# Kernel tuning notes

Measured on AMD Instinct MI355X. Metric: run time of the kernel, lower is better.

The kernel has to match this reference:

```python
import jax, jax.numpy as jnp
import numpy as np

WINDOW = 5  # must be odd so conv 'same' output length == tlength


def setup_inputs() -> dict:
    key = jax.random.key(0)
    tlength = 16777216
    return {"factor": jax.random.normal(key, (tlength,), dtype=jnp.float32)}


def reference(factor):
    window = WINDOW
    # moving average: conv1d with ones kernel, padding=window//2 (== 'same' for odd window)
    w = jnp.ones((window,), dtype=factor.dtype)
    moving_average = jnp.convolve(factor, w, mode='same') / window
    # rate of change: 0 followed by squared consecutive differences
    diffs = (moving_average[:-1] - moving_average[1:]) ** 2
    change = jnp.concatenate([jnp.zeros((1,), dtype=factor.dtype), diffs])
    change = change / jnp.sum(change)
    # power-weighted elementwise scaling
    return (1.0 - change) ** 5 * factor
```

## Files before the change

kernel.cpp:

```cpp
#include <hip/hip_runtime.h>


__device__ __forceinline__ float change_term(const float* __restrict__ f, long long i, long long n) {
    if (i < 1) return 0.0f;
    float a = (i >= 3)    ? f[i - 3] : 0.0f;
    float b = (i + 2 < n) ? f[i + 2] : 0.0f;
    float d = a - b;
    return d * d;
}

__device__ __forceinline__ float pow5(float t) {
    float t2 = t * t;
    float t4 = t2 * t2;
    return t4 * t;
}

__device__ __forceinline__ float vec_terms(float4 p, float4 c, float4 q) {
    float d0 = p.y - c.z;
    float d1 = p.z - c.w;
    float d2 = p.w - q.x;
    float d3 = c.x - q.y;
    return d0 * d0 + d1 * d1 + d2 * d2 + d3 * d3;
}

__global__ void reduce_change_kernel(const float* __restrict__ f, int nvec, long long n,
                                     float* __restrict__ sum_out) {
    const float4* __restrict__ fv = (const float4*)f;
    const int T = gridDim.x * blockDim.x;
    const int tid = blockIdx.x * blockDim.x + threadIdx.x;
    const int M = nvec - 2;
    float acc = 0.0f;

    int idx = tid;
    for (; idx + 3 * T < M; idx += 4 * T) {
        float4 p[4], c[4], q[4];
        #pragma unroll
        for (int u = 0; u < 4; ++u) {
            int v = 1 + idx + u * T;
            p[u] = fv[v - 1];
            c[u] = fv[v];
            q[u] = fv[v + 1];
        }
        #pragma unroll
        for (int u = 0; u < 4; ++u)
            acc += vec_terms(p[u], c[u], q[u]);
    }
    for (; idx < M; idx += T) {
        int v = 1 + idx;
        acc += vec_terms(fv[v - 1], fv[v], fv[v + 1]);
    }
    if (tid == 0) {
        #pragma unroll
        for (int k = 0; k < 4; ++k) acc += change_term(f, k, n);
        long long j0 = n - 4;
        #pragma unroll
        for (int k = 0; k < 4; ++k) acc += change_term(f, j0 + k, n);
    }

    #pragma unroll
    for (int off = 32; off > 0; off >>= 1)
        acc += __shfl_down(acc, off, 64);
    __shared__ float smem[4];
    int lane = threadIdx.x & 63;
    int wave = threadIdx.x >> 6;
    if (lane == 0) smem[wave] = acc;
    __syncthreads();
    if (threadIdx.x == 0) {
        float s = smem[0] + smem[1] + smem[2] + smem[3];
        atomicAdd(sum_out, s);
    }
}

__device__ __forceinline__ float4 vec_out(float4 p, float4 c, float4 q, float inv) {
    float d0 = p.y - c.z;
    float d1 = p.z - c.w;
    float d2 = p.w - q.x;
    float d3 = c.x - q.y;
    float4 o;
    o.x = pow5(1.0f - d0 * d0 * inv) * c.x;
    o.y = pow5(1.0f - d1 * d1 * inv) * c.y;
    o.z = pow5(1.0f - d2 * d2 * inv) * c.z;
    o.w = pow5(1.0f - d3 * d3 * inv) * c.w;
    return o;
}

__global__ void finalize_kernel(const float* __restrict__ f, int nvec, long long n,
                                const float* __restrict__ sum_in,
                                float* __restrict__ out) {
    const float4* __restrict__ fv = (const float4*)f;
    float4* __restrict__ ov = (float4*)out;
    const int M = nvec - 2;
    const int T = (M + 1) >> 1;
    int tid = blockIdx.x * blockDim.x + threadIdx.x;
    if (tid < T) {
        int v1 = 1 + tid;
        bool has2 = (tid + T) < M;
        int v2 = has2 ? (1 + tid + T) : v1;
        float4 p1 = fv[v1 - 1], c1 = fv[v1], q1 = fv[v1 + 1];
        float4 p2 = fv[v2 - 1], c2 = fv[v2], q2 = fv[v2 + 1];
        float inv = 1.0f / *sum_in;
        ov[v1] = vec_out(p1, c1, q1, inv);
        if (has2) ov[v2] = vec_out(p2, c2, q2, inv);
    }
    if (tid == 0) {
        float inv = 1.0f / *sum_in;
        #pragma unroll
        for (int k = 0; k < 4; ++k) {
            float cge = change_term(f, k, n) * inv;
            out[k] = pow5(1.0f - cge) * f[k];
        }
        long long j0 = n - 4;
        #pragma unroll
        for (int k = 0; k < 4; ++k) {
            long long j = j0 + k;
            float cge = change_term(f, j, n) * inv;
            out[j] = pow5(1.0f - cge) * f[j];
        }
    }
}

extern "C" void kernel_launch(void* const* d_in, const int* in_sizes, int n_in,
                              void* d_out, int out_size, void* d_ws, size_t ws_size,
                              hipStream_t stream) {
    const float* f = (const float*)d_in[0];
    float* out = (float*)d_out;
    float* sum_ws = (float*)d_ws;
    long long n = (long long)in_sizes[0];
    int nvec = (int)(n / 4);

    hipMemsetAsync(d_ws, 0, sizeof(float), stream);

    const int block = 256;
    reduce_change_kernel<<<1024, block, 0, stream>>>(f, nvec, n, sum_ws);

    int M = nvec - 2;
    int T = (M + 1) >> 1;
    int fgrid = (T + block - 1) / block;
    finalize_kernel<<<fgrid, block, 0, stream>>>(f, nvec, n, sum_ws, out);
}
```

Before: 128.4 us.

## Fuse reduction and finalize into one kernel with a software grid barrier

Merges the sum-of-squared-differences reduction and the output scaling pass into one persistent kernel. Blocks synchronise through an atomic counter spin-wait once the sum is accumulated. This removes a kernel launch and lets each block reread the input it just touched, which may still sit in cache. The cost is a spin barrier that relies on all 1024 blocks being co-resident. The finalize pass also now uses the grid-stride loop instead of a one-shot grid.

```diff
diff --git a/kernel.cpp b/kernel.cpp
--- a/kernel.cpp
+++ b/kernel.cpp
@@ -1,5 +1,8 @@
 #include <hip/hip_runtime.h>
 
+
+#define GRID_BLOCKS 1024
+#define BLOCK 256
 
 __device__ __forceinline__ float change_term(const float* __restrict__ f, long long i, long long n) {
     if (i < 1) return 0.0f;
@@ -23,14 +26,30 @@
     return d0 * d0 + d1 * d1 + d2 * d2 + d3 * d3;
 }
 
-__global__ void reduce_change_kernel(const float* __restrict__ f, int nvec, long long n,
-                                     float* __restrict__ sum_out) {
+__device__ __forceinline__ float4 vec_out(float4 p, float4 c, float4 q, float inv) {
+    float d0 = p.y - c.z;
+    float d1 = p.z - c.w;
+    float d2 = p.w - q.x;
+    float d3 = c.x - q.y;
+    float4 o;
+    o.x = pow5(1.0f - d0 * d0 * inv) * c.x;
+    o.y = pow5(1.0f - d1 * d1 * inv) * c.y;
+    o.z = pow5(1.0f - d2 * d2 * inv) * c.z;
+    o.w = pow5(1.0f - d3 * d3 * inv) * c.w;
+    return o;
+}
+
+__global__ __launch_bounds__(BLOCK, 4)
+void fused_kernel(const float* __restrict__ f, int nvec, long long n,
+                  float* __restrict__ sum_ws, int* __restrict__ cnt_ws,
+                  float* __restrict__ out) {
     const float4* __restrict__ fv = (const float4*)f;
-    const int T = gridDim.x * blockDim.x;
-    const int tid = blockIdx.x * blockDim.x + threadIdx.x;
+    float4* __restrict__ ov = (float4*)out;
+    const int T = GRID_BLOCKS * BLOCK;
+    const int tid = blockIdx.x * BLOCK + threadIdx.x;
     const int M = nvec - 2;
+
     float acc = 0.0f;
-
     int idx = tid;
     for (; idx + 3 * T < M; idx += 4 * T) {
         float4 p[4], c[4], q[4];
@@ -61,49 +80,44 @@
     for (int off = 32; off > 0; off >>= 1)
         acc += __shfl_down(acc, off, 64);
     __shared__ float smem[4];
+    __shared__ float s_total;
     int lane = threadIdx.x & 63;
     int wave = threadIdx.x >> 6;
     if (lane == 0) smem[wave] = acc;
     __syncthreads();
+
     if (threadIdx.x == 0) {
         float s = smem[0] + smem[1] + smem[2] + smem[3];
-        atomicAdd(sum_out, s);
+        atomicAdd(sum_ws, s);
+        __threadfence();
+        atomicAdd(cnt_ws, 1);
+        while (atomicAdd(cnt_ws, 0) < GRID_BLOCKS) {
+            __builtin_amdgcn_s_sleep(2);
+        }
+        s_total = atomicAdd(sum_ws, 0.0f);
     }
-}
+    __syncthreads();
+    float inv = 1.0f / s_total;
 
-__device__ __forceinline__ float4 vec_out(float4 p, float4 c, float4 q, float inv) {
-    float d0 = p.y - c.z;
-    float d1 = p.z - c.w;
-    float d2 = p.w - q.x;
-    float d3 = c.x - q.y;
-    float4 o;
-    o.x = pow5(1.0f - d0 * d0 * inv) * c.x;
-    o.y = pow5(1.0f - d1 * d1 * inv) * c.y;
-    o.z = pow5(1.0f - d2 * d2 * inv) * c.z;
-    o.w = pow5(1.0f - d3 * d3 * inv) * c.w;
-    return o;
-}
-
-__global__ void finalize_kernel(const float* __restrict__ f, int nvec, long long n,
-                                const float* __restrict__ sum_in,
-                                float* __restrict__ out) {
-    const float4* __restrict__ fv = (const float4*)f;
-    float4* __restrict__ ov = (float4*)out;
-    const int M = nvec - 2;
-    const int T = (M + 1) >> 1;
-    int tid = blockIdx.x * blockDim.x + threadIdx.x;
-    if (tid < T) {
-        int v1 = 1 + tid;
-        bool has2 = (tid + T) < M;
-        int v2 = has2 ? (1 + tid + T) : v1;
-        float4 p1 = fv[v1 - 1], c1 = fv[v1], q1 = fv[v1 + 1];
-        float4 p2 = fv[v2 - 1], c2 = fv[v2], q2 = fv[v2 + 1];
-        float inv = 1.0f / *sum_in;
-        ov[v1] = vec_out(p1, c1, q1, inv);
-        if (has2) ov[v2] = vec_out(p2, c2, q2, inv);
+    idx = tid;
+    for (; idx + 3 * T < M; idx += 4 * T) {
+        float4 p[4], c[4], q[4];
+        #pragma unroll
+        for (int u = 0; u < 4; ++u) {
+            int v = 1 + idx + u * T;
+            p[u] = fv[v - 1];
+            c[u] = fv[v];
+            q[u] = fv[v + 1];
+        }
+        #pragma unroll
+        for (int u = 0; u < 4; ++u)
+            ov[1 + idx + u * T] = vec_out(p[u], c[u], q[u], inv);
+    }
+    for (; idx < M; idx += T) {
+        int v = 1 + idx;
+        ov[v] = vec_out(fv[v - 1], fv[v], fv[v + 1], inv);
     }
     if (tid == 0) {
-        float inv = 1.0f / *sum_in;
         #pragma unroll
         for (int k = 0; k < 4; ++k) {
             float cge = change_term(f, k, n) * inv;
@@ -125,16 +139,11 @@
     const float* f = (const float*)d_in[0];
     float* out = (float*)d_out;
     float* sum_ws = (float*)d_ws;
+    int* cnt_ws = (int*)((char*)d_ws + sizeof(float));
     long long n = (long long)in_sizes[0];
     int nvec = (int)(n / 4);
 
-    hipMemsetAsync(d_ws, 0, sizeof(float), stream);
+    hipMemsetAsync(d_ws, 0, 2 * sizeof(float), stream);
 
-    const int block = 256;
-    reduce_change_kernel<<<1024, block, 0, stream>>>(f, nvec, n, sum_ws);
-
-    int M = nvec - 2;
-    int T = (M + 1) >> 1;
-    int fgrid = (T + block - 1) / block;
-    finalize_kernel<<<fgrid, block, 0, stream>>>(f, nvec, n, sum_ws, out);
+    fused_kernel<<<GRID_BLOCKS, BLOCK, 0, stream>>>(f, nvec, n, sum_ws, cnt_ws, out);
 }
```

After: 272.1 us. 2.12x slower.

## Spread reduction atomics over buckets, double reduce grid, use nontemporal output stores

Applied to the files above, without the earlier changes.

The reduce kernel now accumulates block partials into 16 cache-line-spaced buckets instead of a single float, and its grid grows from 1024 to 2048 blocks. The finalize kernel sums the buckets before inverting. Output stores become nontemporal vector stores to avoid polluting cache. Launch bounds are added. The aim is to cut contention on one atomic address and streaming-store overhead, at the cost of a slightly larger memset and 16 extra loads per thread.

```diff
diff --git a/kernel.cpp b/kernel.cpp
--- a/kernel.cpp
+++ b/kernel.cpp
@@ -1,5 +1,12 @@
 #include <hip/hip_runtime.h>
 
+
+#define BLOCK 256
+#define RGRID 2048
+#define NBUCKET 16
+#define BUCKET_STRIDE 64
+
+typedef __attribute__((ext_vector_type(4))) float vfloat4;
 
 __device__ __forceinline__ float change_term(const float* __restrict__ f, long long i, long long n) {
     if (i < 1) return 0.0f;
@@ -23,11 +30,25 @@
     return d0 * d0 + d1 * d1 + d2 * d2 + d3 * d3;
 }
 
-__global__ void reduce_change_kernel(const float* __restrict__ f, int nvec, long long n,
-                                     float* __restrict__ sum_out) {
+__device__ __forceinline__ vfloat4 vec_out(float4 p, float4 c, float4 q, float inv) {
+    float d0 = p.y - c.z;
+    float d1 = p.z - c.w;
+    float d2 = p.w - q.x;
+    float d3 = c.x - q.y;
+    vfloat4 o;
+    o.x = pow5(1.0f - d0 * d0 * inv) * c.x;
+    o.y = pow5(1.0f - d1 * d1 * inv) * c.y;
+    o.z = pow5(1.0f - d2 * d2 * inv) * c.z;
+    o.w = pow5(1.0f - d3 * d3 * inv) * c.w;
+    return o;
+}
+
+__global__ __launch_bounds__(BLOCK)
+void reduce_change_kernel(const float* __restrict__ f, int nvec, long long n,
+                          float* __restrict__ sum_out) {
     const float4* __restrict__ fv = (const float4*)f;
-    const int T = gridDim.x * blockDim.x;
-    const int tid = blockIdx.x * blockDim.x + threadIdx.x;
+    const int T = RGRID * BLOCK;
+    const int tid = blockIdx.x * BLOCK + threadIdx.x;
     const int M = nvec - 2;
     float acc = 0.0f;
 
@@ -67,43 +88,38 @@
     __syncthreads();
     if (threadIdx.x == 0) {
         float s = smem[0] + smem[1] + smem[2] + smem[3];
-        atomicAdd(sum_out, s);
+        atomicAdd(&sum_out[(blockIdx.x & (NBUCKET - 1)) * BUCKET_STRIDE], s);
     }
 }
 
-__device__ __forceinline__ float4 vec_out(float4 p, float4 c, float4 q, float inv) {
-    float d0 = p.y - c.z;
-    float d1 = p.z - c.w;
-    float d2 = p.w - q.x;
-    float d3 = c.x - q.y;
-    float4 o;
-    o.x = pow5(1.0f - d0 * d0 * inv) * c.x;
-    o.y = pow5(1.0f - d1 * d1 * inv) * c.y;
-    o.z = pow5(1.0f - d2 * d2 * inv) * c.z;
-    o.w = pow5(1.0f - d3 * d3 * inv) * c.w;
-    return o;
+__device__ __forceinline__ float bucket_sum(const float* __restrict__ sum_in) {
+    float s = 0.0f;
+    #pragma unroll
+    for (int b = 0; b < NBUCKET; ++b) s += sum_in[b * BUCKET_STRIDE];
+    return s;
 }
 
-__global__ void finalize_kernel(const float* __restrict__ f, int nvec, long long n,
-                                const float* __restrict__ sum_in,
-                                float* __restrict__ out) {
+__global__ __launch_bounds__(BLOCK)
+void finalize_kernel(const float* __restrict__ f, int nvec, long long n,
+                     const float* __restrict__ sum_in,
+                     float* __restrict__ out) {
     const float4* __restrict__ fv = (const float4*)f;
-    float4* __restrict__ ov = (float4*)out;
+    vfloat4* __restrict__ ov = (vfloat4*)out;
     const int M = nvec - 2;
     const int T = (M + 1) >> 1;
-    int tid = blockIdx.x * blockDim.x + threadIdx.x;
+    int tid = blockIdx.x * BLOCK + threadIdx.x;
     if (tid < T) {
         int v1 = 1 + tid;
         bool has2 = (tid + T) < M;
         int v2 = has2 ? (1 + tid + T) : v1;
         float4 p1 = fv[v1 - 1], c1 = fv[v1], q1 = fv[v1 + 1];
         float4 p2 = fv[v2 - 1], c2 = fv[v2], q2 = fv[v2 + 1];
-        float inv = 1.0f / *sum_in;
-        ov[v1] = vec_out(p1, c1, q1, inv);
-        if (has2) ov[v2] = vec_out(p2, c2, q2, inv);
+        float inv = 1.0f / bucket_sum(sum_in);
+        __builtin_nontemporal_store(vec_out(p1, c1, q1, inv), &ov[v1]);
+        if (has2) __builtin_nontemporal_store(vec_out(p2, c2, q2, inv), &ov[v2]);
     }
     if (tid == 0) {
-        float inv = 1.0f / *sum_in;
+        float inv = 1.0f / bucket_sum(sum_in);
         #pragma unroll
         for (int k = 0; k < 4; ++k) {
             float cge = change_term(f, k, n) * inv;
@@ -128,13 +144,12 @@
     long long n = (long long)in_sizes[0];
     int nvec = (int)(n / 4);
 
-    hipMemsetAsync(d_ws, 0, sizeof(float), stream);
+    (void)hipMemsetAsync(d_ws, 0, NBUCKET * BUCKET_STRIDE * sizeof(float), stream);
 
-    const int block = 256;
-    reduce_change_kernel<<<1024, block, 0, stream>>>(f, nvec, n, sum_ws);
+    reduce_change_kernel<<<RGRID, BLOCK, 0, stream>>>(f, nvec, n, sum_ws);
 
     int M = nvec - 2;
     int T = (M + 1) >> 1;
-    int fgrid = (T + block - 1) / block;
-    finalize_kernel<<<fgrid, block, 0, stream>>>(f, nvec, n, sum_ws, out);
+    int fgrid = (T + BLOCK - 1) / BLOCK;
+    finalize_kernel<<<fgrid, BLOCK, 0, stream>>>(f, nvec, n, sum_ws, out);
 }
```

Result: faster. 119.1 us (-7.3%).
